# Kernel tuning notes

Measured on AMD Instinct MI355X. Metric: run time of the kernel, lower is better.

Reference implementation:

```python
import jax, jax.numpy as jnp
import numpy as np

N = 50000
E = 1600000
D_IN = 128
D_OUT = 128


def setup_inputs() -> dict:
    key = jax.random.key(0)
    k1, k2, k3, k4 = jax.random.split(key, 4)
    x = jax.random.normal(k1, (N, D_IN), dtype=jnp.float32)
    edge_index = jax.random.randint(k2, (2, E), 0, N, dtype=jnp.int64)
    # Linear(in_channels, out_channels) params (torch layout: W [out, in])
    bound = 1.0 / np.sqrt(D_IN)
    W = jax.random.uniform(k3, (D_OUT, D_IN), minval=-bound, maxval=bound, dtype=jnp.float32)
    b = jax.random.uniform(k4, (D_OUT,), minval=-bound, maxval=bound, dtype=jnp.float32)
    return {"x": x, "edge_index": edge_index, "W": W, "b": b}


def reference(x, edge_index, W, b):
    src, dst = edge_index[0], edge_index[1]
    # degree of each node as a source: tg.utils.degree(edge_index[0])
    deg = jax.ops.segment_sum(jnp.ones((E,), dtype=x.dtype), src, num_segments=N)
    norm = jnp.sqrt(deg + 1.0)[:, None]  # [N, 1]
    xn = x / norm
    # message passing with self_loop=True: scatter-add into x itself (out=x)
    agg = xn + jax.ops.segment_sum(xn[src], dst, num_segments=N)  # [N, D_IN]
    h = agg / norm
    return h @ W.T + b
```

## Files before the change

### kernel.cpp

```cpp
#include <hip/hip_runtime.h>

#define NN 50000
#define NE 1600000
#define D 128
#define RPB 40
#define NRS 4
#define RNG 12500
#define NC 32
#define CHUNK 50000
#define NC2 64
#define CHUNK2 25000
#define NBS 196

#define WS_INV  0
#define WS_CNT  204800
#define WS_OFF  409600
#define WS_BSUM 610304
#define WS_WT   614400
#define WS_PDST 679936
#define WS_PSRC 13479936
#define WS_CSR  16679936
#define WS_XNB  679936

__global__ __launch_bounds__(1024) void fused_pre(const int* __restrict__ ei,
                                                  const float* __restrict__ W,
                                                  unsigned short* __restrict__ psrc,
                                                  int* __restrict__ pdst,
                                                  float* __restrict__ Wt) {
    __shared__ int h[RNG];
    int bid = blockIdx.x;
    if (bid < 128) {
        int r = bid >> 5, c = bid & 31;
        int lo = r * RNG;
        for (int j = threadIdx.x; j < RNG; j += 1024) h[j] = 0;
        __syncthreads();
        const int* s = ei + c * CHUNK;
        for (int i = threadIdx.x; i < CHUNK; i += 1024) {
            int k = s[i] - lo;
            if ((unsigned)k < RNG) atomicAdd(&h[k], 1);
        }
        __syncthreads();
        unsigned short* p = psrc + (size_t)bid * RNG;
        for (int j = threadIdx.x; j < RNG; j += 1024) p[j] = (unsigned short)h[j];
    } else if (bid < 384) {
        int b2 = bid - 128;
        int r = b2 >> 6, c = b2 & 63;
        int lo = r * RNG;
        for (int j = threadIdx.x; j < RNG; j += 1024) h[j] = 0;
        __syncthreads();
        const int* d = ei + NE + c * CHUNK2;
        for (int i = threadIdx.x; i < CHUNK2; i += 1024) {
            int k = d[i] - lo;
            if ((unsigned)k < RNG) atomicAdd(&h[k], 1);
        }
        __syncthreads();
        int* p = pdst + (size_t)b2 * RNG;
        for (int j = threadIdx.x; j < RNG; j += 1024) p[j] = h[j];
    } else {
        int i = (bid - 384) * 1024 + threadIdx.x;
        int c = i >> 7, k = i & 127;
        Wt[k * D + c] = W[i];
    }
}

__global__ __launch_bounds__(256) void reduce_scan(const unsigned short* __restrict__ psrc,
                                                   const int* __restrict__ pdst,
                                                   float* __restrict__ inv,
                                                   int* __restrict__ cnt,
                                                   int* __restrict__ off,
                                                   int* __restrict__ bsum) {
    __shared__ int sh[256];
    int tid = threadIdx.x;
    int k = blockIdx.x * 256 + tid;
    int t = 0;
    if (k < NN) {
        int r = k / RNG, j = k - r * RNG;
        size_t bs = (size_t)(r * NC) * RNG + j;
        int s = 0;
#pragma unroll 8
        for (int c = 0; c < NC; ++c) s += psrc[bs + (size_t)c * RNG];
        size_t bd = (size_t)(r * NC2) * RNG + j;
#pragma unroll 8
        for (int c = 0; c < NC2; ++c) t += pdst[bd + (size_t)c * RNG];
        inv[k] = rsqrtf((float)s + 1.0f);
        cnt[k] = t;
    }
    sh[tid] = t;
    __syncthreads();
    for (int d = 1; d < 256; d <<= 1) {
        int v = (tid >= d) ? sh[tid - d] : 0;
        __syncthreads();
        sh[tid] += v;
        __syncthreads();
    }
    if (k < NN) off[k] = sh[tid] - t;
    if (tid == 255) bsum[blockIdx.x] = sh[255];
}

__global__ void scan_chunks(int* __restrict__ pdst, int* __restrict__ off,
                            const int* __restrict__ bsum) {
    int k = blockIdx.x * blockDim.x + threadIdx.x;
    if (k >= NN) return;
    int bi = k >> 8;
    int top = 0;
    for (int c = 0; c < bi; ++c) top += bsum[c];
    int run = off[k] + top;
    off[k] = run;
    int r = k / RNG, j = k - r * RNG;
    size_t base = (size_t)(r * NC2) * RNG + j;
#pragma unroll 8
    for (int c = 0; c < NC2; ++c) {
        size_t p = base + (size_t)c * RNG;
        int v = pdst[p];
        pdst[p] = run;
        run += v;
    }
}

__global__ __launch_bounds__(1024) void fill_sorted(const int* __restrict__ ei,
                                                    const int* __restrict__ bases,
                                                    unsigned short* __restrict__ csr) {
    __shared__ int cur[RNG];
    int r = blockIdx.x >> 6, c = blockIdx.x & 63;
    int lo = r * RNG;
    const int* bslice = bases + (size_t)blockIdx.x * RNG;
    for (int j = threadIdx.x; j < RNG; j += 1024) cur[j] = bslice[j];
    __syncthreads();
    const int* s = ei + c * CHUNK2;
    const int* d = ei + NE + c * CHUNK2;
    for (int i = threadIdx.x; i < CHUNK2; i += 1024) {
        int kd = d[i] - lo;
        if ((unsigned)kd < RNG) {
            int pos = atomicAdd(&cur[kd], 1);
            csr[pos] = (unsigned short)s[i];
        }
    }
}

__device__ __forceinline__ unsigned bf16_rne(float f) {
    unsigned u = __float_as_uint(f);
    return (u + 0x7fffu + ((u >> 16) & 1u)) >> 16;
}
__global__ void scale_kernel(const float* __restrict__ x, const float* __restrict__ inv,
                             unsigned* __restrict__ xnb4) {
    int i = blockIdx.x * blockDim.x + threadIdx.x;
    if (i >= NN * 16) return;
    int row = i >> 4;
    float w = inv[row];
    const float4* src = (const float4*)(x + (size_t)i * 8);
    float4 a = src[0], bq = src[1];
    uint4 o;
    o.x = bf16_rne(a.x * w)  | (bf16_rne(a.y * w) << 16);
    o.y = bf16_rne(a.z * w)  | (bf16_rne(a.w * w) << 16);
    o.z = bf16_rne(bq.x * w) | (bf16_rne(bq.y * w) << 16);
    o.w = bf16_rne(bq.z * w) | (bf16_rne(bq.w * w) << 16);
    ((uint4*)xnb4)[i] = o;
}

#define ACC2(u) do { \
    ax += __uint_as_float((u).x << 16); \
    ay += __uint_as_float((u).x & 0xffff0000u); \
    az += __uint_as_float((u).y << 16); \
    aw += __uint_as_float((u).y & 0xffff0000u); } while (0)

__global__ __launch_bounds__(256) void gather_kernel(const unsigned* __restrict__ xnb,
                                                     const float* __restrict__ inv,
                                                     const int* __restrict__ off,
                                                     const int* __restrict__ cnt,
                                                     const unsigned short* __restrict__ csr,
                                                     float* __restrict__ out) {
    int wid = (blockIdx.x * blockDim.x + threadIdx.x) >> 6;
    if (wid >= NN) return;
    int lane = threadIdx.x & 63;
    int half = lane >> 5;
    int col4 = lane & 31;

    float ax = 0.f, ay = 0.f, az = 0.f, aw = 0.f;
    const uint2* xb = (const uint2*)xnb;
    if (half == 0) {
        uint2 u = xb[(size_t)wid * 32 + col4];
        ACC2(u);
    }
    int n = cnt[wid];
    const unsigned short* row = csr + off[wid];
    int i = half;
    for (; i + 14 < n; i += 16) {
        int s0 = row[i],      s1 = row[i + 2],  s2 = row[i + 4],  s3 = row[i + 6];
        int s4 = row[i + 8],  s5 = row[i + 10], s6 = row[i + 12], s7 = row[i + 14];
        uint2 u0 = xb[(size_t)s0 * 32 + col4];
        uint2 u1 = xb[(size_t)s1 * 32 + col4];
        uint2 u2 = xb[(size_t)s2 * 32 + col4];
        uint2 u3 = xb[(size_t)s3 * 32 + col4];
        uint2 u4 = xb[(size_t)s4 * 32 + col4];
        uint2 u5 = xb[(size_t)s5 * 32 + col4];
        uint2 u6 = xb[(size_t)s6 * 32 + col4];
        uint2 u7 = xb[(size_t)s7 * 32 + col4];
        ACC2(u0); ACC2(u1); ACC2(u2); ACC2(u3);
        ACC2(u4); ACC2(u5); ACC2(u6); ACC2(u7);
    }
    for (; i + 6 < n; i += 8) {
        int s0 = row[i], s1 = row[i + 2], s2 = row[i + 4], s3 = row[i + 6];
        uint2 u0 = xb[(size_t)s0 * 32 + col4];
        uint2 u1 = xb[(size_t)s1 * 32 + col4];
        uint2 u2 = xb[(size_t)s2 * 32 + col4];
        uint2 u3 = xb[(size_t)s3 * 32 + col4];
        ACC2(u0); ACC2(u1); ACC2(u2); ACC2(u3);
    }
    for (; i < n; i += 2) {
        int s = row[i];
        uint2 u = xb[(size_t)s * 32 + col4];
        ACC2(u);
    }
    ax += __shfl_xor(ax, 32, 64);
    ay += __shfl_xor(ay, 32, 64);
    az += __shfl_xor(az, 32, 64);
    aw += __shfl_xor(aw, 32, 64);
    if (half == 0) {
        float wn = inv[wid];
        float4 o;
        o.x = ax * wn; o.y = ay * wn; o.z = az * wn; o.w = aw * wn;
        ((float4*)(out + (size_t)wid * D))[col4] = o;
    }
}

__global__ __launch_bounds__(256) void gemm_kernel(float* io, const float* __restrict__ Wt,
                                                   const float* __restrict__ b) {
    __shared__ float h[RPB][D];
    int r0 = blockIdx.x * RPB;

    const float4* src4 = (const float4*)(io + (size_t)r0 * D);
    for (int t = threadIdx.x; t < RPB * D / 4; t += 256) {
        ((float4*)h)[t] = src4[t];
    }
    __syncthreads();

    int c = threadIdx.x & 127;
    int rh = threadIdx.x >> 7;
    float acc[20];
#pragma unroll
    for (int j = 0; j < 20; ++j) acc[j] = 0.0f;

    for (int k0 = 0; k0 < D; k0 += 4) {
        float w0 = Wt[(k0 + 0) * D + c];
        float w1 = Wt[(k0 + 1) * D + c];
        float w2 = Wt[(k0 + 2) * D + c];
        float w3 = Wt[(k0 + 3) * D + c];
#pragma unroll
        for (int j = 0; j < 20; ++j) {
            float4 hv = *(const float4*)&h[rh * 20 + j][k0];
            acc[j] += hv.x * w0 + hv.y * w1 + hv.z * w2 + hv.w * w3;
        }
    }

    float bc = b[c];
#pragma unroll
    for (int j = 0; j < 20; ++j) {
        io[(size_t)(r0 + rh * 20 + j) * D + c] = acc[j] + bc;
    }
}

extern "C" void kernel_launch(void* const* d_in, const int* in_sizes, int n_in,
                              void* d_out, int out_size, void* d_ws, size_t ws_size,
                              hipStream_t stream) {
    const float* x  = (const float*)d_in[0];
    const int*   ei = (const int*)d_in[1];
    const float* W  = (const float*)d_in[2];
    const float* b  = (const float*)d_in[3];
    float* out = (float*)d_out;

    char* ws = (char*)d_ws;
    float*          inv  = (float*)         (ws + WS_INV);
    int*            cnt  = (int*)           (ws + WS_CNT);
    int*            off  = (int*)           (ws + WS_OFF);
    int*            bsum = (int*)           (ws + WS_BSUM);
    float*          Wt   = (float*)         (ws + WS_WT);
    int*            pdst = (int*)           (ws + WS_PDST);
    unsigned short* psrc = (unsigned short*)(ws + WS_PSRC);
    unsigned short* csr  = (unsigned short*)(ws + WS_CSR);
    unsigned*       xnb  = (unsigned*)      (ws + WS_XNB);

    fused_pre<<<400, 1024, 0, stream>>>(ei, W, psrc, pdst, Wt);
    reduce_scan<<<NBS, 256, 0, stream>>>(psrc, pdst, inv, cnt, off, bsum);
    scan_chunks<<<(NN + 255) / 256, 256, 0, stream>>>(pdst, off, bsum);
    fill_sorted<<<NRS * NC2, 1024, 0, stream>>>(ei, pdst, csr);
    scale_kernel<<<(NN * 16 + 255) / 256, 256, 0, stream>>>(x, inv, xnb);
    gather_kernel<<<(NN * 64 + 255) / 256, 256, 0, stream>>>(xnb, inv, off, cnt, csr, out);
    gemm_kernel<<<NN / RPB, 256, 0, stream>>>(out, Wt, b);
}
```

Measured before the change: 164.7 us.

## Pack degree histograms as 16-bit pairs covering all nodes per block

Measured after the change: 175.1 us. 6.3% more time.

```diff
diff --git a/kernel.cpp b/kernel.cpp
--- a/kernel.cpp
+++ b/kernel.cpp
@@ -4,12 +4,11 @@
 #define NE 1600000
 #define D 128
 #define RPB 40
-#define NRS 4
-#define RNG 12500
-#define NC 32
-#define CHUNK 50000
-#define NC2 64
-#define CHUNK2 25000
+#define NW 25000
+#define NCS 32
+#define CHUNK_S 50000
+#define NCD 32
+#define CHUNK_D 50000
 #define NBS 196
 
 #define WS_INV  0
@@ -17,54 +16,50 @@
 #define WS_OFF  409600
 #define WS_BSUM 610304
 #define WS_WT   614400
-#define WS_PDST 679936
-#define WS_PSRC 13479936
-#define WS_CSR  16679936
-#define WS_XNB  679936
+#define WS_A    679936
+#define WS_B    3879936
+#define WS_C    7079936
+#define WS_D    13479936
 
 __global__ __launch_bounds__(1024) void fused_pre(const int* __restrict__ ei,
                                                   const float* __restrict__ W,
-                                                  unsigned short* __restrict__ psrc,
-                                                  int* __restrict__ pdst,
+                                                  unsigned* __restrict__ psrc_p,
+                                                  unsigned* __restrict__ pdst_p,
                                                   float* __restrict__ Wt) {
-    __shared__ int h[RNG];
+    __shared__ unsigned h[NW];
     int bid = blockIdx.x;
-    if (bid < 128) {
-        int r = bid >> 5, c = bid & 31;
-        int lo = r * RNG;
-        for (int j = threadIdx.x; j < RNG; j += 1024) h[j] = 0;
-        __syncthreads();
-        const int* s = ei + c * CHUNK;
-        for (int i = threadIdx.x; i < CHUNK; i += 1024) {
-            int k = s[i] - lo;
-            if ((unsigned)k < RNG) atomicAdd(&h[k], 1);
-        }
-        __syncthreads();
-        unsigned short* p = psrc + (size_t)bid * RNG;
-        for (int j = threadIdx.x; j < RNG; j += 1024) p[j] = (unsigned short)h[j];
-    } else if (bid < 384) {
-        int b2 = bid - 128;
-        int r = b2 >> 6, c = b2 & 63;
-        int lo = r * RNG;
-        for (int j = threadIdx.x; j < RNG; j += 1024) h[j] = 0;
-        __syncthreads();
-        const int* d = ei + NE + c * CHUNK2;
-        for (int i = threadIdx.x; i < CHUNK2; i += 1024) {
-            int k = d[i] - lo;
-            if ((unsigned)k < RNG) atomicAdd(&h[k], 1);
-        }
-        __syncthreads();
-        int* p = pdst + (size_t)b2 * RNG;
-        for (int j = threadIdx.x; j < RNG; j += 1024) p[j] = h[j];
+    if (bid < NCS) {
+        for (int j = threadIdx.x; j < NW; j += 1024) h[j] = 0;
+        __syncthreads();
+        const int* s = ei + bid * CHUNK_S;
+        for (int i = threadIdx.x; i < CHUNK_S; i += 1024) {
+            int v = s[i];
+            atomicAdd(&h[v >> 1], 1u << ((v & 1) << 4));
+        }
+        __syncthreads();
+        unsigned* p = psrc_p + (size_t)bid * NW;
+        for (int j = threadIdx.x; j < NW; j += 1024) p[j] = h[j];
+    } else if (bid < NCS + NCD) {
+        int c = bid - NCS;
+        for (int j = threadIdx.x; j < NW; j += 1024) h[j] = 0;
+        __syncthreads();
+        const int* d = ei + NE + c * CHUNK_D;
+        for (int i = threadIdx.x; i < CHUNK_D; i += 1024) {
+            int v = d[i];
+            atomicAdd(&h[v >> 1], 1u << ((v & 1) << 4));
+        }
+        __syncthreads();
+        unsigned* p = pdst_p + (size_t)c * NW;
+        for (int j = threadIdx.x; j < NW; j += 1024) p[j] = h[j];
     } else {
-        int i = (bid - 384) * 1024 + threadIdx.x;
+        int i = (bid - NCS - NCD) * 1024 + threadIdx.x;
         int c = i >> 7, k = i & 127;
         Wt[k * D + c] = W[i];
     }
 }
 
-__global__ __launch_bounds__(256) void reduce_scan(const unsigned short* __restrict__ psrc,
-                                                   const int* __restrict__ pdst,
+__global__ __launch_bounds__(256) void reduce_scan(const unsigned* __restrict__ psrc_p,
+                                                   const unsigned* __restrict__ pdst_p,
                                                    float* __restrict__ inv,
                                                    int* __restrict__ cnt,
                                                    int* __restrict__ off,
@@ -74,14 +69,12 @@
     int k = blockIdx.x * 256 + tid;
     int t = 0;
     if (k < NN) {
-        int r = k / RNG, j = k - r * RNG;
-        size_t bs = (size_t)(r * NC) * RNG + j;
+        int j = k >> 1, shf = (k & 1) << 4;
         int s = 0;
 #pragma unroll 8
-        for (int c = 0; c < NC; ++c) s += psrc[bs + (size_t)c * RNG];
-        size_t bd = (size_t)(r * NC2) * RNG + j;
+        for (int c = 0; c < NCS; ++c) s += (psrc_p[(size_t)c * NW + j] >> shf) & 0xffffu;
 #pragma unroll 8
-        for (int c = 0; c < NC2; ++c) t += pdst[bd + (size_t)c * RNG];
+        for (int c = 0; c < NCD; ++c) t += (pdst_p[(size_t)c * NW + j] >> shf) & 0xffffu;
         inv[k] = rsqrtf((float)s + 1.0f);
         cnt[k] = t;
     }
@@ -97,22 +90,31 @@
     if (tid == 255) bsum[blockIdx.x] = sh[255];
 }
 
-__global__ void scan_chunks(int* __restrict__ pdst, int* __restrict__ off,
-                            const int* __restrict__ bsum) {
-    int k = blockIdx.x * blockDim.x + threadIdx.x;
+__global__ __launch_bounds__(256) void scan_chunks(const unsigned* __restrict__ pdst_p,
+                                                   int* __restrict__ bases,
+                                                   int* __restrict__ off,
+                                                   const int* __restrict__ bsum) {
+    __shared__ int sb[256];
+    int tid = threadIdx.x;
+    int bi = blockIdx.x;
+    sb[tid] = (tid < bi) ? bsum[tid] : 0;
+    __syncthreads();
+    for (int d = 1; d < 256; d <<= 1) {
+        int v = (tid >= d) ? sb[tid - d] : 0;
+        __syncthreads();
+        sb[tid] += v;
+        __syncthreads();
+    }
+    int top = sb[255];
+    int k = bi * 256 + tid;
     if (k >= NN) return;
-    int bi = k >> 8;
-    int top = 0;
-    for (int c = 0; c < bi; ++c) top += bsum[c];
     int run = off[k] + top;
     off[k] = run;
-    int r = k / RNG, j = k - r * RNG;
-    size_t base = (size_t)(r * NC2) * RNG + j;
+    int j = k >> 1, shf = (k & 1) << 4;
 #pragma unroll 8
-    for (int c = 0; c < NC2; ++c) {
-        size_t p = base + (size_t)c * RNG;
-        int v = pdst[p];
-        pdst[p] = run;
+    for (int c = 0; c < NCD; ++c) {
+        int v = (pdst_p[(size_t)c * NW + j] >> shf) & 0xffffu;
+        bases[(size_t)c * NN + k] = run;
         run += v;
     }
 }
@@ -120,17 +122,17 @@
 __global__ __launch_bounds__(1024) void fill_sorted(const int* __restrict__ ei,
                                                     const int* __restrict__ bases,
                                                     unsigned short* __restrict__ csr) {
-    __shared__ int cur[RNG];
-    int r = blockIdx.x >> 6, c = blockIdx.x & 63;
-    int lo = r * RNG;
-    const int* bslice = bases + (size_t)blockIdx.x * RNG;
-    for (int j = threadIdx.x; j < RNG; j += 1024) cur[j] = bslice[j];
-    __syncthreads();
-    const int* s = ei + c * CHUNK2;
-    const int* d = ei + NE + c * CHUNK2;
-    for (int i = threadIdx.x; i < CHUNK2; i += 1024) {
+    __shared__ int cur[NW];
+    int R = blockIdx.x >> 5, c = blockIdx.x & 31;
+    int lo = R * NW;
+    const int* bslice = bases + (size_t)c * NN + lo;
+    for (int j = threadIdx.x; j < NW; j += 1024) cur[j] = bslice[j];
+    __syncthreads();
+    const int* s = ei + c * CHUNK_D;
+    const int* d = ei + NE + c * CHUNK_D;
+    for (int i = threadIdx.x; i < CHUNK_D; i += 1024) {
         int kd = d[i] - lo;
-        if ((unsigned)kd < RNG) {
+        if ((unsigned)kd < NW) {
             int pos = atomicAdd(&cur[kd], 1);
             csr[pos] = (unsigned short)s[i];
         }
@@ -269,20 +271,21 @@
     float* out = (float*)d_out;
 
     char* ws = (char*)d_ws;
-    float*          inv  = (float*)         (ws + WS_INV);
-    int*            cnt  = (int*)           (ws + WS_CNT);
-    int*            off  = (int*)           (ws + WS_OFF);
-    int*            bsum = (int*)           (ws + WS_BSUM);
-    float*          Wt   = (float*)         (ws + WS_WT);
-    int*            pdst = (int*)           (ws + WS_PDST);
-    unsigned short* psrc = (unsigned short*)(ws + WS_PSRC);
-    unsigned short* csr  = (unsigned short*)(ws + WS_CSR);
-    unsigned*       xnb  = (unsigned*)      (ws + WS_XNB);
-
-    fused_pre<<<400, 1024, 0, stream>>>(ei, W, psrc, pdst, Wt);
-    reduce_scan<<<NBS, 256, 0, stream>>>(psrc, pdst, inv, cnt, off, bsum);
-    scan_chunks<<<(NN + 255) / 256, 256, 0, stream>>>(pdst, off, bsum);
-    fill_sorted<<<NRS * NC2, 1024, 0, stream>>>(ei, pdst, csr);
+    float*          inv    = (float*)         (ws + WS_INV);
+    int*            cnt    = (int*)           (ws + WS_CNT);
+    int*            off    = (int*)           (ws + WS_OFF);
+    int*            bsum   = (int*)           (ws + WS_BSUM);
+    float*          Wt     = (float*)         (ws + WS_WT);
+    unsigned*       psrc_p = (unsigned*)      (ws + WS_A);
+    unsigned short* csr    = (unsigned short*)(ws + WS_A);
+    unsigned*       pdst_p = (unsigned*)      (ws + WS_B);
+    int*            bases  = (int*)           (ws + WS_C);
+    unsigned*       xnb    = (unsigned*)      (ws + WS_B);
+
+    fused_pre<<<NCS + NCD + 16, 1024, 0, stream>>>(ei, W, psrc_p, pdst_p, Wt);
+    reduce_scan<<<NBS, 256, 0, stream>>>(psrc_p, pdst_p, inv, cnt, off, bsum);
+    scan_chunks<<<NBS, 256, 0, stream>>>(pdst_p, bases, off, bsum);
+    fill_sorted<<<64, 1024, 0, stream>>>(ei, bases, csr);
     scale_kernel<<<(NN * 16 + 255) / 256, 256, 0, stream>>>(x, inv, xnb);
     gather_kernel<<<(NN * 64 + 255) / 256, 256, 0, stream>>>(xnb, inv, off, cnt, csr, out);
     gemm_kernel<<<NN / RPB, 256, 0, stream>>>(out, Wt, b);
```

## Merge CSR-building preprocessing kernels into one cooperative kernel with grid syncs

Applied to the files above, without the earlier changes.

Result: slower. 289.3 us (+75.7%).

```diff
diff --git a/kernel.cpp b/kernel.cpp
--- a/kernel.cpp
+++ b/kernel.cpp
@@ -1,160 +1,172 @@
 #include <hip/hip_runtime.h>
+#include <hip/hip_cooperative_groups.h>
+
+namespace cg = cooperative_groups;
 
 #define NN 50000
 #define NE 1600000
 #define D 128
 #define RPB 40
-#define NRS 4
-#define RNG 12500
-#define NC 32
-#define CHUNK 50000
-#define NC2 64
-#define CHUNK2 25000
-#define NBS 196
-
-#define WS_INV  0
-#define WS_CNT  204800
-#define WS_OFF  409600
-#define WS_BSUM 610304
-#define WS_WT   614400
-#define WS_PDST 679936
-#define WS_PSRC 13479936
-#define WS_CSR  16679936
-#define WS_XNB  679936
-
-__global__ __launch_bounds__(1024) void fused_pre(const int* __restrict__ ei,
-                                                  const float* __restrict__ W,
-                                                  unsigned short* __restrict__ psrc,
-                                                  int* __restrict__ pdst,
-                                                  float* __restrict__ Wt) {
-    __shared__ int h[RNG];
-    int bid = blockIdx.x;
-    if (bid < 128) {
-        int r = bid >> 5, c = bid & 31;
-        int lo = r * RNG;
-        for (int j = threadIdx.x; j < RNG; j += 1024) h[j] = 0;
-        __syncthreads();
-        const int* s = ei + c * CHUNK;
-        for (int i = threadIdx.x; i < CHUNK; i += 1024) {
-            int k = s[i] - lo;
-            if ((unsigned)k < RNG) atomicAdd(&h[k], 1);
-        }
-        __syncthreads();
-        unsigned short* p = psrc + (size_t)bid * RNG;
-        for (int j = threadIdx.x; j < RNG; j += 1024) p[j] = (unsigned short)h[j];
-    } else if (bid < 384) {
-        int b2 = bid - 128;
-        int r = b2 >> 6, c = b2 & 63;
-        int lo = r * RNG;
-        for (int j = threadIdx.x; j < RNG; j += 1024) h[j] = 0;
-        __syncthreads();
-        const int* d = ei + NE + c * CHUNK2;
-        for (int i = threadIdx.x; i < CHUNK2; i += 1024) {
-            int k = d[i] - lo;
-            if ((unsigned)k < RNG) atomicAdd(&h[k], 1);
-        }
-        __syncthreads();
-        int* p = pdst + (size_t)b2 * RNG;
-        for (int j = threadIdx.x; j < RNG; j += 1024) p[j] = h[j];
-    } else {
-        int i = (bid - 384) * 1024 + threadIdx.x;
-        int c = i >> 7, k = i & 127;
-        Wt[k * D + c] = W[i];
-    }
-}
-
-__global__ __launch_bounds__(256) void reduce_scan(const unsigned short* __restrict__ psrc,
-                                                   const int* __restrict__ pdst,
-                                                   float* __restrict__ inv,
-                                                   int* __restrict__ cnt,
-                                                   int* __restrict__ off,
-                                                   int* __restrict__ bsum) {
-    __shared__ int sh[256];
-    int tid = threadIdx.x;
-    int k = blockIdx.x * 256 + tid;
-    int t = 0;
-    if (k < NN) {
-        int r = k / RNG, j = k - r * RNG;
-        size_t bs = (size_t)(r * NC) * RNG + j;
-        int s = 0;
-#pragma unroll 8
-        for (int c = 0; c < NC; ++c) s += psrc[bs + (size_t)c * RNG];
-        size_t bd = (size_t)(r * NC2) * RNG + j;
-#pragma unroll 8
-        for (int c = 0; c < NC2; ++c) t += pdst[bd + (size_t)c * RNG];
-        inv[k] = rsqrtf((float)s + 1.0f);
-        cnt[k] = t;
-    }
-    sh[tid] = t;
-    __syncthreads();
-    for (int d = 1; d < 256; d <<= 1) {
-        int v = (tid >= d) ? sh[tid - d] : 0;
-        __syncthreads();
-        sh[tid] += v;
-        __syncthreads();
-    }
-    if (k < NN) off[k] = sh[tid] - t;
-    if (tid == 255) bsum[blockIdx.x] = sh[255];
-}
-
-__global__ void scan_chunks(int* __restrict__ pdst, int* __restrict__ off,
-                            const int* __restrict__ bsum) {
-    int k = blockIdx.x * blockDim.x + threadIdx.x;
-    if (k >= NN) return;
-    int bi = k >> 8;
-    int top = 0;
-    for (int c = 0; c < bi; ++c) top += bsum[c];
-    int run = off[k] + top;
-    off[k] = run;
-    int r = k / RNG, j = k - r * RNG;
-    size_t base = (size_t)(r * NC2) * RNG + j;
-#pragma unroll 8
-    for (int c = 0; c < NC2; ++c) {
-        size_t p = base + (size_t)c * RNG;
-        int v = pdst[p];
-        pdst[p] = run;
-        run += v;
-    }
-}
-
-__global__ __launch_bounds__(1024) void fill_sorted(const int* __restrict__ ei,
-                                                    const int* __restrict__ bases,
-                                                    unsigned short* __restrict__ csr) {
-    __shared__ int cur[RNG];
-    int r = blockIdx.x >> 6, c = blockIdx.x & 63;
-    int lo = r * RNG;
-    const int* bslice = bases + (size_t)blockIdx.x * RNG;
-    for (int j = threadIdx.x; j < RNG; j += 1024) cur[j] = bslice[j];
-    __syncthreads();
-    const int* s = ei + c * CHUNK2;
-    const int* d = ei + NE + c * CHUNK2;
-    for (int i = threadIdx.x; i < CHUNK2; i += 1024) {
-        int kd = d[i] - lo;
-        if ((unsigned)kd < RNG) {
-            int pos = atomicAdd(&cur[kd], 1);
-            csr[pos] = (unsigned short)s[i];
-        }
-    }
-}
+
+#define WS_INV   0
+#define WS_CNT   204800
+#define WS_OFF   409600
+#define WS_BSUM  610304
+#define WS_WT    614400
+#define WS_A     679936
+#define WS_B     3879936
+#define WS_C     10279936
 
 __device__ __forceinline__ unsigned bf16_rne(float f) {
     unsigned u = __float_as_uint(f);
     return (u + 0x7fffu + ((u >> 16) & 1u)) >> 16;
 }
-__global__ void scale_kernel(const float* __restrict__ x, const float* __restrict__ inv,
-                             unsigned* __restrict__ xnb4) {
-    int i = blockIdx.x * blockDim.x + threadIdx.x;
-    if (i >= NN * 16) return;
-    int row = i >> 4;
-    float w = inv[row];
-    const float4* src = (const float4*)(x + (size_t)i * 8);
-    float4 a = src[0], bq = src[1];
-    uint4 o;
-    o.x = bf16_rne(a.x * w)  | (bf16_rne(a.y * w) << 16);
-    o.y = bf16_rne(a.z * w)  | (bf16_rne(a.w * w) << 16);
-    o.z = bf16_rne(bq.x * w) | (bf16_rne(bq.y * w) << 16);
-    o.w = bf16_rne(bq.z * w) | (bf16_rne(bq.w * w) << 16);
-    ((uint4*)xnb4)[i] = o;
+
+__global__ __launch_bounds__(1024) void coop_prep(const int* __restrict__ ei,
+                                                  const float* __restrict__ x,
+                                                  const float* __restrict__ W,
+                                                  float* __restrict__ inv,
+                                                  int* __restrict__ cnt,
+                                                  int* __restrict__ off,
+                                                  int* __restrict__ bsum,
+                                                  float* __restrict__ Wt,
+                                                  unsigned* __restrict__ psrc8,
+                                                  unsigned* __restrict__ pdst8,
+                                                  unsigned* __restrict__ bases16,
+                                                  unsigned short* __restrict__ csr,
+                                                  unsigned* __restrict__ xnb) {
+    __shared__ unsigned lds[12500];
+    cg::grid_group grid = cg::this_grid();
+    int bid = blockIdx.x, tid = threadIdx.x;
+
+    if (bid < 64) {
+        for (int j = tid; j < 12500; j += 1024) lds[j] = 0;
+        __syncthreads();
+        const int* s = ei + bid * 25000;
+        for (int i = tid; i < 25000; i += 1024) {
+            int v = s[i];
+            atomicAdd(&lds[v >> 2], 1u << ((v & 3) << 3));
+        }
+        __syncthreads();
+        unsigned* p = psrc8 + (size_t)bid * 12500;
+        for (int j = tid; j < 12500; j += 1024) p[j] = lds[j];
+    } else if (bid < 192) {
+        int c = bid - 64;
+        for (int j = tid; j < 12500; j += 1024) lds[j] = 0;
+        __syncthreads();
+        const int* d = ei + NE + c * 12500;
+        for (int i = tid; i < 12500; i += 1024) {
+            int v = d[i];
+            atomicAdd(&lds[v >> 2], 1u << ((v & 3) << 3));
+        }
+        __syncthreads();
+        unsigned* p = pdst8 + (size_t)c * 12500;
+        for (int j = tid; j < 12500; j += 1024) p[j] = lds[j];
+    } else {
+        int i = (bid - 192) * 1024 + tid;
+        Wt[(i & 127) * D + (i >> 7)] = W[i];
+    }
+    grid.sync();
+
+    if (bid < 13) {
+        int w = bid * 1024 + tid;
+        int t0 = 0, t1 = 0, t2 = 0, t3 = 0;
+        if (w < 12500) {
+            int d0 = 0, d1 = 0, d2 = 0, d3 = 0;
+            for (int c = 0; c < 64; ++c) {
+                unsigned v = psrc8[(size_t)c * 12500 + w];
+                d0 += v & 255; d1 += (v >> 8) & 255; d2 += (v >> 16) & 255; d3 += v >> 24;
+            }
+            for (int c = 0; c < 128; ++c) {
+                unsigned v = pdst8[(size_t)c * 12500 + w];
+                t0 += v & 255; t1 += (v >> 8) & 255; t2 += (v >> 16) & 255; t3 += v >> 24;
+            }
+            int k = w * 4;
+            inv[k]     = rsqrtf((float)d0 + 1.0f);
+            inv[k + 1] = rsqrtf((float)d1 + 1.0f);
+            inv[k + 2] = rsqrtf((float)d2 + 1.0f);
+            inv[k + 3] = rsqrtf((float)d3 + 1.0f);
+            cnt[k] = t0; cnt[k + 1] = t1; cnt[k + 2] = t2; cnt[k + 3] = t3;
+        }
+        int tsum = t0 + t1 + t2 + t3;
+        int* sh = (int*)lds;
+        sh[tid] = tsum;
+        __syncthreads();
+        for (int dd = 1; dd < 1024; dd <<= 1) {
+            int v = (tid >= dd) ? sh[tid - dd] : 0;
+            __syncthreads();
+            sh[tid] += v;
+            __syncthreads();
+        }
+        if (w < 12500) {
+            int ex = sh[tid] - tsum;
+            int k = w * 4;
+            off[k]     = ex;
+            off[k + 1] = ex + t0;
+            off[k + 2] = ex + t0 + t1;
+            off[k + 3] = ex + t0 + t1 + t2;
+        }
+        if (tid == 1023) bsum[bid] = sh[1023];
+    }
+    grid.sync();
+
+    if (bid < 13) {
+        int w = bid * 1024 + tid;
+        if (w < 12500) {
+            int top = 0;
+            for (int c = 0; c < bid; ++c) top += bsum[c];
+            int k = w * 4;
+            off[k] += top; off[k + 1] += top; off[k + 2] += top; off[k + 3] += top;
+            unsigned r0 = 0, r1 = 0, r2 = 0, r3 = 0;
+            for (int c = 0; c < 64; ++c) {
+                unsigned va = pdst8[(size_t)(2 * c) * 12500 + w];
+                unsigned vb = pdst8[(size_t)(2 * c + 1) * 12500 + w];
+                bases16[(size_t)c * 25000 + w * 2]     = r0 | (r1 << 16);
+                bases16[(size_t)c * 25000 + w * 2 + 1] = r2 | (r3 << 16);
+                r0 += (va & 255) + (vb & 255);
+                r1 += ((va >> 8) & 255) + ((vb >> 8) & 255);
+                r2 += ((va >> 16) & 255) + ((vb >> 16) & 255);
+                r3 += (va >> 24) + (vb >> 24);
+            }
+        }
+    }
+    grid.sync();
+
+    if (bid < 128) {
+        int R = bid >> 6, c = bid & 63;
+        int lo = R * 25000;
+        const unsigned* bs = bases16 + (size_t)c * 25000 + (lo >> 1);
+        for (int j = tid; j < 12500; j += 1024) lds[j] = bs[j];
+        __syncthreads();
+        const int* s = ei + c * 25000;
+        const int* d = ei + NE + c * 25000;
+        for (int i = tid; i < 25000; i += 1024) {
+            int dv = d[i];
+            int kd = dv - lo;
+            if ((unsigned)kd < 25000u) {
+                unsigned old = atomicAdd(&lds[kd >> 1], 1u << ((kd & 1) << 4));
+                int rel = (old >> ((kd & 1) << 4)) & 0xffff;
+                csr[off[dv] + rel] = (unsigned short)s[i];
+            }
+        }
+    }
+    grid.sync();
+
+    {
+        int stride = 208 * 1024;
+        for (int i = bid * 1024 + tid; i < NN * 16; i += stride) {
+            int row = i >> 4;
+            float wq = inv[row];
+            const float4* src = (const float4*)(x + (size_t)i * 8);
+            float4 a = src[0], bq = src[1];
+            uint4 o;
+            o.x = bf16_rne(a.x * wq)  | (bf16_rne(a.y * wq) << 16);
+            o.y = bf16_rne(a.z * wq)  | (bf16_rne(a.w * wq) << 16);
+            o.z = bf16_rne(bq.x * wq) | (bf16_rne(bq.y * wq) << 16);
+            o.w = bf16_rne(bq.z * wq) | (bf16_rne(bq.w * wq) << 16);
+            ((uint4*)xnb)[i] = o;
+        }
+    }
 }
 
 #define ACC2(u) do { \
@@ -262,28 +274,29 @@
 extern "C" void kernel_launch(void* const* d_in, const int* in_sizes, int n_in,
                               void* d_out, int out_size, void* d_ws, size_t ws_size,
                               hipStream_t stream) {
+    const int*   ei = (const int*)d_in[1];
     const float* x  = (const float*)d_in[0];
-    const int*   ei = (const int*)d_in[1];
     const float* W  = (const float*)d_in[2];
     const float* b  = (const float*)d_in[3];
     float* out = (float*)d_out;
 
     char* ws = (char*)d_ws;
-    float*          inv  = (float*)         (ws + WS_INV);
-    int*            cnt  = (int*)           (ws + WS_CNT);
-    int*            off  = (int*)           (ws + WS_OFF);
-    int*            bsum = (int*)           (ws + WS_BSUM);
-    float*          Wt   = (float*)         (ws + WS_WT);
-    int*            pdst = (int*)           (ws + WS_PDST);
-    unsigned short* psrc = (unsigned short*)(ws + WS_PSRC);
-    unsigned short* csr  = (unsigned short*)(ws + WS_CSR);
-    unsigned*       xnb  = (unsigned*)      (ws + WS_XNB);
-
-    fused_pre<<<400, 1024, 0, stream>>>(ei, W, psrc, pdst, Wt);
-    reduce_scan<<<NBS, 256, 0, stream>>>(psrc, pdst, inv, cnt, off, bsum);
-    scan_chunks<<<(NN + 255) / 256, 256, 0, stream>>>(pdst, off, bsum);
-    fill_sorted<<<NRS * NC2, 1024, 0, stream>>>(ei, pdst, csr);
-    scale_kernel<<<(NN * 16 + 255) / 256, 256, 0, stream>>>(x, inv, xnb);
+    float*          inv     = (float*)         (ws + WS_INV);
+    int*            cnt     = (int*)           (ws + WS_CNT);
+    int*            off     = (int*)           (ws + WS_OFF);
+    int*            bsum    = (int*)           (ws + WS_BSUM);
+    float*          Wt      = (float*)         (ws + WS_WT);
+    unsigned*       psrc8   = (unsigned*)      (ws + WS_A);
+    unsigned short* csr     = (unsigned short*)(ws + WS_A);
+    unsigned*       pdst8   = (unsigned*)      (ws + WS_B);
+    unsigned*       bases16 = (unsigned*)      (ws + WS_C);
+    unsigned*       xnb     = (unsigned*)      (ws + WS_B);
+
+    void* args[] = {(void*)&ei, (void*)&x, (void*)&W, (void*)&inv, (void*)&cnt,
+                    (void*)&off, (void*)&bsum, (void*)&Wt, (void*)&psrc8,
+                    (void*)&pdst8, (void*)&bases16, (void*)&csr, (void*)&xnb};
+    hipLaunchCooperativeKernel((void*)coop_prep, dim3(208), dim3(1024), args, 0, stream);
+
     gather_kernel<<<(NN * 64 + 255) / 256, 256, 0, stream>>>(xnb, inv, off, cnt, csr, out);
     gemm_kernel<<<NN / RPB, 256, 0, stream>>>(out, Wt, b);
 }
```
